# Performance work log

Measured on AMD Instinct MI355X. Metric: run time of the kernel, lower is better.

Reference implementation:

```python
import jax, jax.numpy as jnp
import numpy as np

C = 512        # channels
H = 8          # num_heads
GN_ATTN = 32   # GroupNorm32 groups
GN_CONV = 8    # Conv1dBlock GroupNorm groups


def _mish(x):
    return x * jnp.tanh(jax.nn.softplus(x))


def _group_norm(x, w, b, groups, eps=1e-5):
    # x: (B, C, T); normalize per group over (C//groups, T) in fp32
    B, Cc, T = x.shape
    xf = x.astype(jnp.float32).reshape(B, groups, Cc // groups, T)
    mean = xf.mean(axis=(2, 3), keepdims=True)
    var = xf.var(axis=(2, 3), keepdims=True)
    xn = ((xf - mean) * jax.lax.rsqrt(var + eps)).reshape(B, Cc, T)
    return (xn * w[None, :, None] + b[None, :, None]).astype(x.dtype)


def _conv1d_same(x, w, b):
    # x: (B, Cin, T), w: (Cout, Cin, K)
    y = jax.lax.conv_general_dilated(
        x, w, window_strides=(1,), padding='SAME',
        dimension_numbers=('NCH', 'OIH', 'NCH'))
    return y + b[None, :, None]


def setup_inputs() -> dict:
    key = jax.random.key(0)
    ks = jax.random.split(key, 12)
    B, T = 8, 1024
    s_qkv = 1.0 / np.sqrt(C * 2)
    s_proj = 1.0 / np.sqrt(C * 4)
    return {
        'x':       jax.random.normal(ks[0], (B, C, T), jnp.float32),
        'gn_w':    jnp.ones((C,), jnp.float32),
        'gn_b':    jnp.zeros((C,), jnp.float32),
        'wqkv':    jax.random.normal(ks[1], (3 * C, C, 2), jnp.float32) * s_qkv,
        'bqkv':    jnp.zeros((3 * C,), jnp.float32),
        'gnq_w':   jnp.ones((3 * C,), jnp.float32),
        'gnq_b':   jnp.zeros((3 * C,), jnp.float32),
        'wproj':   jax.random.normal(ks[2], (C, C, 4), jnp.float32) * s_proj,
        'bproj':   jnp.zeros((C,), jnp.float32),
        'gnp_w':   jnp.ones((C,), jnp.float32),
        'gnp_b':   jnp.zeros((C,), jnp.float32),
    }


def _qkv_attention(qkv):
    # qkv: (B*H, 3*dh, T)
    ch = qkv.shape[1] // 3
    q, k, v = jnp.split(qkv, 3, axis=1)
    scale = 1.0 / np.sqrt(np.sqrt(ch))
    # (bh, t, s) full score matrix, softmax in fp32 as original
    weight = jnp.einsum('bct,bcs->bts', q * scale, k * scale)
    weight = jax.nn.softmax(weight.astype(jnp.float32), axis=-1).astype(weight.dtype)
    return jnp.einsum('bts,bcs->bct', weight, v)


def reference(x, gn_w, gn_b, wqkv, bqkv, gnq_w, gnq_b, wproj, bproj, gnp_w, gnp_b):
    B, Cc, T = x.shape
    # norm -> qkv Conv1dBlock (conv -> GN(8) -> Mish)
    h = _group_norm(x, gn_w, gn_b, GN_ATTN)
    qkv = _mish(_group_norm(_conv1d_same(h, wqkv, bqkv), gnq_w, gnq_b, GN_CONV))
    # heads: (B, 3C, T) -> (B*H, 3C/H, T)
    qkv = qkv.reshape(B * H, (3 * Cc) // H, T)
    a = _qkv_attention(qkv)                       # (B*H, C/H, T)
    a = a.reshape(B, Cc, T)
    # proj Conv1dBlock + residual
    h = _mish(_group_norm(_conv1d_same(a, wproj, bproj), gnp_w, gnp_b, GN_CONV))
    return x + h
```

## Files before the change

kernel.cpp:

```cpp
#include <hip/hip_runtime.h>
#include <hip/hip_bf16.h>
#include <math.h>

#define TID threadIdx.x

constexpr int Cc = 512, Tt = 1024, C3 = 1536;

typedef __attribute__((ext_vector_type(8))) __bf16 bf16x8;
typedef __attribute__((ext_vector_type(4))) float f32x4;

__device__ __forceinline__ void async16(const void* g, void* l) {
  __builtin_amdgcn_global_load_lds(
      (const __attribute__((address_space(1))) unsigned int*)g,
      (__attribute__((address_space(3))) unsigned int*)l, 16, 0, 0);
}

__device__ __forceinline__ unsigned int pack2bf(float a, float b) {
  __hip_bfloat162 h;
  h.x = __float2bfloat16(a);
  h.y = __float2bfloat16(b);
  return *reinterpret_cast<unsigned int*>(&h);
}

__device__ __forceinline__ float bf2f(unsigned short u) {
  unsigned int t = ((unsigned int)u) << 16;
  union { unsigned int i; float f; } c;
  c.i = t;
  return c.f;
}

__device__ __forceinline__ float exp2_hw(float x) {
  float r;
  asm("v_exp_f32 %0, %1" : "=v"(r) : "v"(x));
  return r;
}

__device__ __forceinline__ float mishf(float x) {
  float u = __expf(x);
  float n = u * (u + 2.f);
  float r = x * n * __builtin_amdgcn_rcpf(n + 2.f);
  return (x > 20.f) ? x : r;
}

__device__ __forceinline__ void blockReduce2(float& s, float& ss) {
  #pragma unroll
  for (int off = 32; off > 0; off >>= 1) {
    s  += __shfl_xor(s,  off);
    ss += __shfl_xor(ss, off);
  }
  __shared__ float ls[4], lss[4];
  int w = TID >> 6;
  if ((TID & 63) == 0) { ls[w] = s; lss[w] = ss; }
  __syncthreads();
  s  = ls[0] + ls[1] + ls[2] + ls[3];
  ss = lss[0] + lss[1] + lss[2] + lss[3];
}

__global__ void zero_stats(float* p) { p[TID] = 0.f; }

__global__ __launch_bounds__(256) void zero_pads(__hip_bfloat16* __restrict__ aT) {
  int idx = blockIdx.x * 256 + TID;
  int bb = idx >> 11;
  int task = idx & 2047;
  int prow = task >> 6;
  int col = (task & 63) * 8;
  int P = (prow < 16) ? prow : (1024 + prow);
  uint4 z = {0u, 0u, 0u, 0u};
  *reinterpret_cast<uint4*>(aT + ((size_t)bb * 1056 + P) * 512 + col) = z;
}

__global__ __launch_bounds__(256) void gn1_hT(const float* __restrict__ x,
    const float* __restrict__ w, const float* __restrict__ bv,
    __hip_bfloat16* __restrict__ hT) {
  __shared__ float hs[16][262];
  int blk = blockIdx.x, bb = blk >> 5, g = blk & 31;
  size_t base = ((size_t)bb * Cc + g * 16) * Tt;
  const float* xp = x + base;
  float s = 0.f, ss = 0.f;
  for (int i = TID * 4; i < 16 * Tt; i += 1024) {
    float4 v = *reinterpret_cast<const float4*>(xp + i);
    s  += v.x + v.y + v.z + v.w;
    ss += v.x * v.x + v.y * v.y + v.z * v.z + v.w * v.w;
  }
  blockReduce2(s, ss);
  float mean = s * (1.f / 16384.f);
  float rstd = rsqrtf(ss * (1.f / 16384.f) - mean * mean + 1e-5f);

  __hip_bfloat16* ob = hT + (size_t)bb * 1056 * 512 + g * 16;
  for (int tc = 0; tc < 4; ++tc) {
    int tbase = tc * 256;
    __syncthreads();
    for (int task = TID; task < 1024; task += 256) {
      int row = task >> 6, c4 = task & 63;
      int ch = g * 16 + row;
      float sw = w[ch] * rstd;
      float sb = bv[ch] - mean * sw;
      float4 v = *reinterpret_cast<const float4*>(xp + (size_t)row * Tt + tbase + c4 * 4);
      hs[row][c4 * 4 + 0] = v.x * sw + sb;
      hs[row][c4 * 4 + 1] = v.y * sw + sb;
      hs[row][c4 * 4 + 2] = v.z * sw + sb;
      hs[row][c4 * 4 + 3] = v.w * sw + sb;
    }
    __syncthreads();
    for (int task = TID; task < 512; task += 256) {
      int t = task >> 1, half = task & 1;
      int c0 = half * 8;
      uint4 u;
      u.x = pack2bf(hs[c0 + 0][t], hs[c0 + 1][t]);
      u.y = pack2bf(hs[c0 + 2][t], hs[c0 + 3][t]);
      u.z = pack2bf(hs[c0 + 4][t], hs[c0 + 5][t]);
      u.w = pack2bf(hs[c0 + 6][t], hs[c0 + 7][t]);
      *reinterpret_cast<uint4*>(ob + (size_t)(16 + tbase + t) * 512 + c0) = u;
    }
  }
}

__global__ __launch_bounds__(256) void cast_wqkv(const float* __restrict__ wq,
    __hip_bfloat16* __restrict__ A1s) {
  int o = blockIdx.x;
  int ci = TID * 2;
  float4 v = *reinterpret_cast<const float4*>(wq + ((size_t)o * 512 + ci) * 2);
  unsigned int u0 = pack2bf(v.x, v.z);
  unsigned int u1 = pack2bf(v.y, v.w);
  *reinterpret_cast<unsigned int*>(A1s + (size_t)o * 512 + ci) = u0;
  *reinterpret_cast<unsigned int*>(A1s + ((size_t)1536 + o) * 512 + ci) = u1;
}

__global__ __launch_bounds__(256) void cast_wproj(const float* __restrict__ wp,
    __hip_bfloat16* __restrict__ A2) {
  int o = blockIdx.x;
  int ci = TID * 2;
  float4 v0 = *reinterpret_cast<const float4*>(wp + ((size_t)o * 512 + ci) * 4);
  float4 v1 = *reinterpret_cast<const float4*>(wp + ((size_t)o * 512 + ci + 1) * 4);
  const float* a0 = &v0.x;
  const float* a1 = &v1.x;
  #pragma unroll
  for (int j = 0; j < 4; ++j) {
    unsigned int u = pack2bf(a0[j], a1[j]);
    *reinterpret_cast<unsigned int*>(A2 + ((size_t)j * 512 + o) * 512 + ci) = u;
  }
}

__global__ __launch_bounds__(1024, 4) void gemm_s2(const __hip_bfloat16* __restrict__ A1s,
    const __hip_bfloat16* __restrict__ hT, const float* __restrict__ bias,
    __hip_bfloat16* __restrict__ Cout, float* __restrict__ statraw) {
  constexpr int BUF = 41 * 1024;
  __shared__ __align__(16) char lds[2 * BUF];
  int bz = blockIdx.x & 7;
  int inner = blockIdx.x >> 3;
  int t0 = (inner & 3) * 256;
  int og = inner >> 2;
  int o0 = og * 192;
  int wave = TID >> 6, lane = TID & 63;
  int l4 = lane >> 4, r15 = lane & 15;
  int wm = wave >> 2, wn = wave & 3;
  const __hip_bfloat16* hTb = hT + (size_t)bz * 1056 * 512;

  f32x4 acc[3][4];
  f32x4 zz = {0.f, 0.f, 0.f, 0.f};
  #pragma unroll
  for (int m = 0; m < 3; ++m)
    #pragma unroll
    for (int n = 0; n < 4; ++n) acc[m][n] = zz;

  auto stage = [&](int kt, int buf) {
    char* dst = lds + buf * BUF;
    #pragma unroll
    for (int c = 0; c < 3; ++c) {
      int ch = c * 16 + wave;
      if (ch < 41) {
        const __hip_bfloat16* src;
        if (ch < 24) {
          int j = (ch >= 12) ? 1 : 0;
          int rg = ch - j * 12;
          src = A1s + ((size_t)j * 1536 + o0 + rg * 16 + r15) * 512 + kt * 32 + l4 * 8;
        } else {
          int rg = ch - 24;
          src = hTb + (size_t)(16 + t0 + rg * 16 + r15) * 512 + kt * 32 + l4 * 8;
        }
        async16(src, dst + ch * 1024 + lane * 16);
      }
    }
  };

  stage(0, 0);
  __syncthreads();
  for (int kt = 0; kt < 16; ++kt) {
    if (kt + 1 < 16) stage(kt + 1, (kt + 1) & 1);
    char* cur = lds + (kt & 1) * BUF;
    #pragma unroll
    for (int j = 0; j < 2; ++j) {
      bf16x8 af[3], bfr[4];
      #pragma unroll
      for (int m = 0; m < 3; ++m)
        af[m] = *reinterpret_cast<const bf16x8*>(cur + (j * 12 + wm * 3 + m) * 1024 + lane * 16);
      #pragma unroll
      for (int n = 0; n < 4; ++n) {
        int q = (wn * 4 + n) * 16 + r15 + j;
        bfr[n] = *reinterpret_cast<const bf16x8*>(cur + 24 * 1024 + (q >> 4) * 1024 + l4 * 256 + (q & 15) * 16);
      }
      #pragma unroll
      for (int m = 0; m < 3; ++m)
        #pragma unroll
        for (int n = 0; n < 4; ++n)
          acc[m][n] = __builtin_amdgcn_mfma_f32_16x16x32_bf16(af[m], bfr[n], acc[m][n], 0, 0, 0);
    }
    __syncthreads();
  }

  float* sred = reinterpret_cast<float*>(lds);
  #pragma unroll
  for (int m = 0; m < 3; ++m) {
    float s = 0.f, ss2 = 0.f;
    #pragma unroll
    for (int n = 0; n < 4; ++n) {
      int ocol = t0 + (wn * 4 + n) * 16 + r15;
      #pragma unroll
      for (int r = 0; r < 4; ++r) {
        int orow = o0 + (wm * 3 + m) * 16 + l4 * 4 + r;
        float v = acc[m][n][r] + bias[orow];
        Cout[((size_t)bz * C3 + orow) * 1024 + ocol] = __float2bfloat16(v);
        s += v;
        ss2 += v * v;
      }
    }
    #pragma unroll
    for (int off = 1; off < 64; off <<= 1) {
      s   += __shfl_xor(s, off);
      ss2 += __shfl_xor(ss2, off);
    }
    if (lane == 0) {
      sred[(wave * 3 + m) * 2]     = s;
      sred[(wave * 3 + m) * 2 + 1] = ss2;
    }
  }
  __syncthreads();
  if (TID == 0) {
    float S = 0.f, SS = 0.f;
    #pragma unroll
    for (int slot = 0; slot < 48; ++slot) {
      S  += sred[slot * 2];
      SS += sred[slot * 2 + 1];
    }
    int g = bz * 8 + og;
    atomicAdd(&statraw[2 * g],     S);
    atomicAdd(&statraw[2 * g + 1], SS);
  }
}

__global__ __launch_bounds__(256) void gemm_c4b(const __hip_bfloat16* __restrict__ A2,
    const __hip_bfloat16* __restrict__ aT, const float* __restrict__ bias,
    float* __restrict__ Cout, float* __restrict__ statraw) {
  constexpr int BUF = 42 * 1024;
  __shared__ __align__(16) char lds[2 * BUF];
  int bz = blockIdx.x & 7;
  int inner = blockIdx.x >> 3;
  int t0 = (inner & 7) * 128;
  int o0 = (inner >> 3) * 128;
  int wave = TID >> 6, lane = TID & 63;
  int l4 = lane >> 4, r15 = lane & 15;
  int wm = wave >> 1, wn = wave & 1;
  const __hip_bfloat16* aTb = aT + (size_t)bz * 1056 * 512;

  f32x4 acc[4][4];
  f32x4 zz = {0.f, 0.f, 0.f, 0.f};
  #pragma unroll
  for (int m = 0; m < 4; ++m)
    #pragma unroll
    for (int n = 0; n < 4; ++n) acc[m][n] = zz;

  auto stage = [&](int kt, int buf) {
    char* dst = lds + buf * BUF;
    #pragma unroll
    for (int c = 0; c < 11; ++c) {
      int ch = c * 4 + wave;
      if (ch < 42) {
        const __hip_bfloat16* src;
        if (ch < 32) {
          int j = ch >> 3, rg = ch & 7;
          src = A2 + ((size_t)j * 512 + o0 + rg * 16 + r15) * 512 + kt * 32 + l4 * 8;
        } else {
          int rg = ch - 32;
          src = aTb + (size_t)(t0 + rg * 16 + r15) * 512 + kt * 32 + l4 * 8;
        }
        async16(src, dst + ch * 1024 + lane * 16);
      }
    }
  };

  stage(0, 0);
  __syncthreads();
  for (int kt = 0; kt < 16; ++kt) {
    if (kt + 1 < 16) stage(kt + 1, (kt + 1) & 1);
    char* cur = lds + (kt & 1) * BUF;
    #pragma unroll
    for (int j = 0; j < 4; ++j) {
      bf16x8 af[4], bfr[4];
      #pragma unroll
      for (int m = 0; m < 4; ++m)
        af[m] = *reinterpret_cast<const bf16x8*>(cur + (j * 8 + wm * 4 + m) * 1024 + lane * 16);
      #pragma unroll
      for (int n = 0; n < 4; ++n) {
        int q = (wn * 4 + n) * 16 + r15 + j + 15;
        bfr[n] = *reinterpret_cast<const bf16x8*>(cur + 32 * 1024 + (q >> 4) * 1024 + l4 * 256 + (q & 15) * 16);
      }
      #pragma unroll
      for (int m = 0; m < 4; ++m)
        #pragma unroll
        for (int n = 0; n < 4; ++n)
          acc[m][n] = __builtin_amdgcn_mfma_f32_16x16x32_bf16(af[m], bfr[n], acc[m][n], 0, 0, 0);
    }
    __syncthreads();
  }

  float* sred = reinterpret_cast<float*>(lds);
  #pragma unroll
  for (int m = 0; m < 4; ++m) {
    float s = 0.f, ss2 = 0.f;
    #pragma unroll
    for (int n = 0; n < 4; ++n) {
      int ocol = t0 + (wn * 4 + n) * 16 + r15;
      #pragma unroll
      for (int r = 0; r < 4; ++r) {
        int orow = o0 + (wm * 4 + m) * 16 + l4 * 4 + r;
        float v = acc[m][n][r] + bias[orow];
        Cout[((size_t)bz * Cc + orow) * 1024 + ocol] = v;
        s += v;
        ss2 += v * v;
      }
    }
    #pragma unroll
    for (int off = 1; off < 64; off <<= 1) {
      s   += __shfl_xor(s, off);
      ss2 += __shfl_xor(ss2, off);
    }
    if (lane == 0) {
      sred[(wave * 4 + m) * 2]     = s;
      sred[(wave * 4 + m) * 2 + 1] = ss2;
    }
  }
  __syncthreads();
  if (TID < 2) {
    int g0 = o0 >> 6;
    float S = 0.f, SS = 0.f;
    int cnt = 0;
    #pragma unroll
    for (int slot = 0; slot < 16; ++slot) {
      int rc = ((slot >> 3) << 2) + (slot & 3);
      int g = (o0 + rc * 16) >> 6;
      if (g == g0 + (int)TID) {
        S  += sred[slot * 2];
        SS += sred[slot * 2 + 1];
        ++cnt;
      }
    }
    if (cnt) {
      atomicAdd(&statraw[2 * (bz * 8 + g0 + TID)],     S);
      atomicAdd(&statraw[2 * (bz * 8 + g0 + TID) + 1], SS);
    }
  }
}

__global__ __launch_bounds__(256) void gn2_prep(const __hip_bfloat16* __restrict__ qkv,
    const float* __restrict__ straw, const float* __restrict__ w, const float* __restrict__ bv,
    char* __restrict__ qTp, char* __restrict__ kimg, char* __restrict__ vimg) {
  __shared__ unsigned short hbf[192 * 66];
  int tl = blockIdx.x & 15, hb = blockIdx.x >> 4;
  int b = hb >> 3, hd = hb & 7;
  float rs = straw[2 * (b * 8 + hd)], rq = straw[2 * (b * 8 + hd) + 1];
  float mean = rs * (1.f / 196608.f);
  float rstd = rsqrtf(fmaxf(rq * (1.f / 196608.f) - mean * mean, 0.f) + 1e-5f);
  for (int task = TID; task < 768; task += 256) {
    int row = task >> 2, seg = task & 3;
    int ch = hd * 192 + row;
    float sw = w[ch] * rstd;
    float sb = bv[ch] - mean * sw;
    const uint4* src = reinterpret_cast<const uint4*>(
        qkv + ((size_t)(b * C3 + ch)) * 1024 + tl * 64 + seg * 16);
    uint4 u0 = src[0], u1 = src[1];
    unsigned int uu[8] = {u0.x, u0.y, u0.z, u0.w, u1.x, u1.y, u1.z, u1.w};
    unsigned int* dst = reinterpret_cast<unsigned int*>(&hbf[row * 66 + seg * 16]);
    #pragma unroll
    for (int j = 0; j < 8; ++j) {
      float a = mishf(bf2f((unsigned short)(uu[j] & 0xffff)) * sw + sb);
      float c = mishf(bf2f((unsigned short)(uu[j] >> 16)) * sw + sb);
      dst[j] = pack2bf(a, c);
    }
  }
  __syncthreads();
  size_t tileof = ((size_t)hb * 16 + tl) * 8192;
  {
    int t = TID & 63, sel = TID >> 6;
    int img = sel >> 1, half = sel & 1;
    char* obase = (img == 0 ? qTp : kimg) + tileof + (size_t)t * 128;
    #pragma unroll
    for (int cc = 0; cc < 4; ++cc) {
      int chunk = half * 4 + cc;
      uint4 u;
      unsigned int* up = reinterpret_cast<unsigned int*>(&u);
      #pragma unroll
      for (int j = 0; j < 4; ++j) {
        int c = chunk * 8 + j * 2;
        unsigned int lo = hbf[(img * 64 + c) * 66 + t];
        unsigned int hi = hbf[(img * 64 + c + 1) * 66 + t];
        up[j] = lo | (hi << 16);
      }
      int cpos = (img == 0) ? chunk : (chunk ^ (t & 7));
      *reinterpret_cast<uint4*>(obase + cpos * 16) = u;
    }
  }
  {
    int c = TID & 63, qtr = TID >> 6;
    const unsigned int* vrow = reinterpret_cast<const unsigned int*>(&hbf[(128 + c) * 66]);
    char* obase = vimg + tileof + (size_t)c * 128;
    #pragma unroll
    for (int k = 0; k < 2; ++k) {
      int chunk = qtr * 2 + k;
      uint4 u;
      unsigned int* up = reinterpret_cast<unsigned int*>(&u);
      #pragma unroll
      for (int j = 0; j < 4; ++j) up[j] = vrow[chunk * 4 + j];
      *reinterpret_cast<uint4*>(obase + (chunk ^ (c & 7)) * 16) = u;
    }
  }
}

__global__ __launch_bounds__(1024) void attn_mfma6(const char* __restrict__ qTp,
    const char* __restrict__ kimg, const char* __restrict__ vimg,
    __hip_bfloat16* __restrict__ aT) {
  __shared__ __align__(16) char smem[131072];
  char* kbuf0 = smem;
  char* kbuf1 = smem + 16384;
  char* vbuf0 = smem + 32768;
  char* vbuf1 = smem + 49152;
  char* pp    = smem + 65536;
  char* ov    = smem;

  int hb = blockIdx.y;
  int b = hb >> 3, hd = hb & 7;
  int lane = TID & 63, wave = TID >> 6;
  int qt = wave >> 2, qw = wave & 3;
  int l4 = lane >> 4, r15 = lane & 15;
  size_t ibase = (size_t)hb * 16 * 8192;
  const char* ksrc = kimg + ibase;
  const char* vsrc = vimg + ibase;

  async16(ksrc + (size_t)TID * 16, kbuf0 + (size_t)TID * 16);
  async16(vsrc + (size_t)TID * 16, vbuf0 + (size_t)TID * 16);

  bf16x8 aq[2];
  int tg = qw * 16 + r15;
  const char* qrow = qTp + ibase + (size_t)(blockIdx.x * 4 + qt) * 8192 + (size_t)tg * 128;
  aq[0] = *reinterpret_cast<const bf16x8*>(qrow + l4 * 16);
  aq[1] = *reinterpret_cast<const bf16x8*>(qrow + 64 + l4 * 16);
  {
    const float SC = 0.125f * 1.44269504f;
    #pragma unroll
    for (int kk = 0; kk < 2; ++kk) {
      unsigned int* u = reinterpret_cast<unsigned int*>(&aq[kk]);
      #pragma unroll
      for (int j = 0; j < 4; ++j) {
        float lo = bf2f((unsigned short)(u[j] & 0xffff)) * SC;
        float hi = bf2f((unsigned short)(u[j] >> 16)) * SC;
        u[j] = pack2bf(lo, hi);
      }
    }
  }

  f32x4 osum[4];
  f32x4 zz = {0.f, 0.f, 0.f, 0.f};
  #pragma unroll
  for (int cf = 0; cf < 4; ++cf) osum[cf] = zz;
  float mrow[4] = {-1e30f, -1e30f, -1e30f, -1e30f};
  float lrow[4] = {0.f, 0.f, 0.f, 0.f};
  __syncthreads();

  for (int it = 0; it < 8; ++it) {
    char* kcur = (it & 1) ? kbuf1 : kbuf0;
    char* vcur = (it & 1) ? vbuf1 : vbuf0;
    if (it < 7) {
      char* knxt = (it & 1) ? kbuf0 : kbuf1;
      char* vnxt = (it & 1) ? vbuf0 : vbuf1;
      const char* kn = ksrc + (size_t)(it + 1) * 16384;
      const char* vn = vsrc + (size_t)(it + 1) * 16384;
      async16(kn + (size_t)TID * 16, knxt + (size_t)TID * 16);
      async16(vn + (size_t)TID * 16, vnxt + (size_t)TID * 16);
    }
    f32x4 sc[8];
    #pragma unroll
    for (int sf = 0; sf < 8; ++sf) sc[sf] = zz;
    #pragma unroll
    for (int sf = 0; sf < 8; ++sf) {
      int sr = sf * 16 + r15;
      #pragma unroll
      for (int kk = 0; kk < 2; ++kk) {
        bf16x8 bk = *reinterpret_cast<const bf16x8*>(kcur + sr * 128 + (((kk * 4 + l4) ^ (sr & 7)) << 4));
        sc[sf] = __builtin_amdgcn_mfma_f32_16x16x32_bf16(aq[kk], bk, sc[sf], 0, 0, 0);
      }
    }
    float tmax[4];
    #pragma unroll
    for (int r = 0; r < 4; ++r) {
      float m0 = fmaxf(fmaxf(sc[0][r], sc[1][r]), fmaxf(sc[2][r], sc[3][r]));
      float m1 = fmaxf(fmaxf(sc[4][r], sc[5][r]), fmaxf(sc[6][r], sc[7][r]));
      tmax[r] = fmaxf(m0, m1);
    }
    #pragma unroll
    for (int off = 1; off < 16; off <<= 1)
      #pragma unroll
      for (int r = 0; r < 4; ++r) tmax[r] = fmaxf(tmax[r], __shfl_xor(tmax[r], off));
    bool grow = (tmax[0] > mrow[0]) | (tmax[1] > mrow[1]) |
                (tmax[2] > mrow[2]) | (tmax[3] > mrow[3]);
    if (grow) {
      float alpha[4];
      #pragma unroll
      for (int r = 0; r < 4; ++r) {
        float mnew = fmaxf(mrow[r], tmax[r]);
        alpha[r] = exp2_hw(mrow[r] - mnew);
        mrow[r] = mnew;
        lrow[r] *= alpha[r];
      }
      #pragma unroll
      for (int cf = 0; cf < 4; ++cf)
        #pragma unroll
        for (int r = 0; r < 4; ++r) osum[cf][r] *= alpha[r];
    }
    char* pw = pp + wave * 4096;
    float psum[4] = {0.f, 0.f, 0.f, 0.f};
    #pragma unroll
    for (int sf = 0; sf < 8; ++sf) {
      int s = sf * 16 + r15;
      int chunk = s >> 3;
      #pragma unroll
      for (int r = 0; r < 4; ++r) {
        float p = exp2_hw(sc[sf][r] - mrow[r]);
        psum[r] += p;
        int tlc = l4 * 4 + r;
        *reinterpret_cast<__hip_bfloat16*>(pw + tlc * 256 + (((chunk ^ (tlc & 15)) << 4) | ((s & 7) * 2)))
            = __float2bfloat16(p);
      }
    }
    #pragma unroll
    for (int r = 0; r < 4; ++r) lrow[r] += psum[r];
    asm volatile("s_waitcnt lgkmcnt(0)" ::: "memory");
    __builtin_amdgcn_sched_barrier(0);

    bf16x8 pa[4];
    #pragma unroll
    for (int kk2 = 0; kk2 < 4; ++kk2)
      pa[kk2] = *reinterpret_cast<const bf16x8*>(pw + r15 * 256 + (((kk2 * 4 + l4) ^ (r15 & 15)) << 4));
    #pragma unroll
    for (int cf = 0; cf < 4; ++cf) {
      int cr = cf * 16 + r15;
      #pragma unroll
      for (int kk2 = 0; kk2 < 4; ++kk2) {
        bf16x8 bv = *reinterpret_cast<const bf16x8*>(vcur + (kk2 >> 1) * 8192 + cr * 128 +
                                                     ((((kk2 & 1) * 4 + l4) ^ (cr & 7)) << 4));
        osum[cf] = __builtin_amdgcn_mfma_f32_16x16x32_bf16(pa[kk2], bv, osum[cf], 0, 0, 0);
      }
    }
    __syncthreads();
  }

  #pragma unroll
  for (int off = 1; off < 16; off <<= 1)
    #pragma unroll
    for (int r = 0; r < 4; ++r) lrow[r] += __shfl_xor(lrow[r], off);
  float linv[4];
  #pragma unroll
  for (int r = 0; r < 4; ++r) linv[r] = 1.f / lrow[r];

  #pragma unroll
  for (int cf = 0; cf < 4; ++cf) {
    int c = cf * 16 + r15;
    #pragma unroll
    for (int r = 0; r < 4; ++r) {
      int t = qt * 64 + qw * 16 + l4 * 4 + r;
      *reinterpret_cast<__hip_bfloat16*>(ov + t * 128 + ((((c >> 3) ^ (t & 7)) << 4) | ((c & 7) * 2)))
          = __float2bfloat16(osum[cf][r] * linv[r]);
    }
  }
  __syncthreads();
  __hip_bfloat16* ap = aT + ((size_t)b * 1056 + 16 + blockIdx.x * 256) * 512 + hd * 64;
  for (int u = TID; u < 2048; u += 1024) {
    int t = u >> 3, cj = u & 7;
    uint4 o4 = *reinterpret_cast<const uint4*>(ov + t * 128 + ((cj ^ (t & 7)) << 4));
    *reinterpret_cast<uint4*>(ap + (size_t)t * 512 + cj * 8) = o4;
  }
}

__global__ __launch_bounds__(256) void final_kernel(const float* __restrict__ x,
    float* __restrict__ y, const float* __restrict__ straw,
    const float* __restrict__ w, const float* __restrict__ bv) {
  size_t i = ((size_t)blockIdx.x * 256 + TID) * 4;
  int ch = (int)((i >> 10) & (Cc - 1));
  int b = (int)(i >> 19);
  int g = b * 8 + (ch >> 6);
  float rs = straw[2 * g], rq = straw[2 * g + 1];
  float mean = rs * (1.f / 65536.f);
  float rstd = rsqrtf(fmaxf(rq * (1.f / 65536.f) - mean * mean, 0.f) + 1e-5f);
  float sw = w[ch] * rstd;
  float sb = bv[ch] - mean * sw;
  float4 v  = *reinterpret_cast<const float4*>(y + i);
  float4 xv = *reinterpret_cast<const float4*>(x + i);
  v.x = xv.x + mishf(v.x * sw + sb);
  v.y = xv.y + mishf(v.y * sw + sb);
  v.z = xv.z + mishf(v.z * sw + sb);
  v.w = xv.w + mishf(v.w * sw + sb);
  *reinterpret_cast<float4*>(y + i) = v;
}

extern "C" void kernel_launch(void* const* d_in, const int* in_sizes, int n_in,
                              void* d_out, int out_size, void* d_ws, size_t ws_size,
                              hipStream_t stream) {
  const float* x     = (const float*)d_in[0];
  const float* gn_w  = (const float*)d_in[1];
  const float* gn_b  = (const float*)d_in[2];
  const float* wqkv  = (const float*)d_in[3];
  const float* bqkv  = (const float*)d_in[4];
  const float* gnq_w = (const float*)d_in[5];
  const float* gnq_b = (const float*)d_in[6];
  const float* wproj = (const float*)d_in[7];
  const float* bproj = (const float*)d_in[8];
  const float* gnp_w = (const float*)d_in[9];
  const float* gnp_b = (const float*)d_in[10];
  float* out = (float*)d_out;

  char* ws = (char*)d_ws;
  const size_t MB = 1024 * 1024;
  __hip_bfloat16* qkvb = (__hip_bfloat16*)ws;
  __hip_bfloat16* aT   = (__hip_bfloat16*)(ws + 24 * MB);
  __hip_bfloat16* A1s  = (__hip_bfloat16*)(ws + 40 * MB);
  __hip_bfloat16* A2   = (__hip_bfloat16*)(ws + 44 * MB);
  char* vimg = ws + 56 * MB;
  float* st2raw = (float*)(ws + 64 * MB);
  float* st3raw = st2raw + 128;
  __hip_bfloat16* hT = (__hip_bfloat16*)d_out;
  char* qTp  = (char*)d_out;
  char* kimg = (char*)d_out + 8 * MB;

  dim3 blk(256);
  zero_stats<<<1, blk, 0, stream>>>(st2raw);
  zero_pads<<<64, blk, 0, stream>>>(aT);
  zero_pads<<<64, blk, 0, stream>>>(hT);
  cast_wqkv<<<1536, blk, 0, stream>>>(wqkv, A1s);
  gn1_hT<<<256, blk, 0, stream>>>(x, gn_w, gn_b, hT);
  gemm_s2<<<256, dim3(1024), 0, stream>>>(A1s, hT, bqkv, qkvb, st2raw);
  gn2_prep<<<1024, blk, 0, stream>>>(qkvb, st2raw, gnq_w, gnq_b, qTp, kimg, vimg);
  attn_mfma6<<<dim3(4, 64), dim3(1024), 0, stream>>>(qTp, kimg, vimg, aT);
  cast_wproj<<<512, blk, 0, stream>>>(wproj, A2);
  gemm_c4b<<<256, blk, 0, stream>>>(A2, aT, bproj, out, st3raw);
  final_kernel<<<4096, blk, 0, stream>>>(x, out, st3raw, gnp_w, gnp_b);
}
```

Before: 155.5 us.

## Merge prep kernels, retile projection GEMM, add MFMA priority hints in attention

After: 144.0 us. 1.08x faster.

```diff
diff --git a/kernel.cpp b/kernel.cpp
--- a/kernel.cpp
+++ b/kernel.cpp
@@ -56,17 +56,44 @@
   ss = lss[0] + lss[1] + lss[2] + lss[3];
 }
 
-__global__ void zero_stats(float* p) { p[TID] = 0.f; }
-
-__global__ __launch_bounds__(256) void zero_pads(__hip_bfloat16* __restrict__ aT) {
-  int idx = blockIdx.x * 256 + TID;
-  int bb = idx >> 11;
-  int task = idx & 2047;
-  int prow = task >> 6;
-  int col = (task & 63) * 8;
-  int P = (prow < 16) ? prow : (1024 + prow);
-  uint4 z = {0u, 0u, 0u, 0u};
-  *reinterpret_cast<uint4*>(aT + ((size_t)bb * 1056 + P) * 512 + col) = z;
+__global__ __launch_bounds__(256) void prep_misc(const float* __restrict__ wq,
+    const float* __restrict__ wp, __hip_bfloat16* __restrict__ A1s,
+    __hip_bfloat16* __restrict__ A2, __hip_bfloat16* __restrict__ aT,
+    __hip_bfloat16* __restrict__ hT, float* __restrict__ stats) {
+  int bid = blockIdx.x;
+  if (bid < 128) {
+    __hip_bfloat16* dst = (bid < 64) ? aT : hT;
+    int idx = ((bid & 63)) * 256 + TID;
+    int bb = idx >> 11;
+    int task = idx & 2047;
+    int prow = task >> 6;
+    int col = (task & 63) * 8;
+    int P = (prow < 16) ? prow : (1024 + prow);
+    uint4 z = {0u, 0u, 0u, 0u};
+    *reinterpret_cast<uint4*>(dst + ((size_t)bb * 1056 + P) * 512 + col) = z;
+  } else if (bid < 1664) {
+    int o = bid - 128;
+    int ci = TID * 2;
+    float4 v = *reinterpret_cast<const float4*>(wq + ((size_t)o * 512 + ci) * 2);
+    unsigned int u0 = pack2bf(v.x, v.z);
+    unsigned int u1 = pack2bf(v.y, v.w);
+    *reinterpret_cast<unsigned int*>(A1s + (size_t)o * 512 + ci) = u0;
+    *reinterpret_cast<unsigned int*>(A1s + ((size_t)1536 + o) * 512 + ci) = u1;
+  } else if (bid < 2176) {
+    int o = bid - 1664;
+    int ci = TID * 2;
+    float4 v0 = *reinterpret_cast<const float4*>(wp + ((size_t)o * 512 + ci) * 4);
+    float4 v1 = *reinterpret_cast<const float4*>(wp + ((size_t)o * 512 + ci + 1) * 4);
+    const float* a0 = &v0.x;
+    const float* a1 = &v1.x;
+    #pragma unroll
+    for (int j = 0; j < 4; ++j) {
+      unsigned int u = pack2bf(a0[j], a1[j]);
+      *reinterpret_cast<unsigned int*>(A2 + ((size_t)j * 512 + o) * 512 + ci) = u;
+    }
+  } else {
+    stats[TID] = 0.f;
+  }
 }
 
 __global__ __launch_bounds__(256) void gn1_hT(const float* __restrict__ x,
@@ -115,32 +142,6 @@
   }
 }
 
-__global__ __launch_bounds__(256) void cast_wqkv(const float* __restrict__ wq,
-    __hip_bfloat16* __restrict__ A1s) {
-  int o = blockIdx.x;
-  int ci = TID * 2;
-  float4 v = *reinterpret_cast<const float4*>(wq + ((size_t)o * 512 + ci) * 2);
-  unsigned int u0 = pack2bf(v.x, v.z);
-  unsigned int u1 = pack2bf(v.y, v.w);
-  *reinterpret_cast<unsigned int*>(A1s + (size_t)o * 512 + ci) = u0;
-  *reinterpret_cast<unsigned int*>(A1s + ((size_t)1536 + o) * 512 + ci) = u1;
-}
-
-__global__ __launch_bounds__(256) void cast_wproj(const float* __restrict__ wp,
-    __hip_bfloat16* __restrict__ A2) {
-  int o = blockIdx.x;
-  int ci = TID * 2;
-  float4 v0 = *reinterpret_cast<const float4*>(wp + ((size_t)o * 512 + ci) * 4);
-  float4 v1 = *reinterpret_cast<const float4*>(wp + ((size_t)o * 512 + ci + 1) * 4);
-  const float* a0 = &v0.x;
-  const float* a1 = &v1.x;
-  #pragma unroll
-  for (int j = 0; j < 4; ++j) {
-    unsigned int u = pack2bf(a0[j], a1[j]);
-    *reinterpret_cast<unsigned int*>(A2 + ((size_t)j * 512 + o) * 512 + ci) = u;
-  }
-}
-
 __global__ __launch_bounds__(1024, 4) void gemm_s2(const __hip_bfloat16* __restrict__ A1s,
     const __hip_bfloat16* __restrict__ hT, const float* __restrict__ bias,
     __hip_bfloat16* __restrict__ Cout, float* __restrict__ statraw) {
@@ -248,18 +249,17 @@
   }
 }
 
-__global__ __launch_bounds__(256) void gemm_c4b(const __hip_bfloat16* __restrict__ A2,
+__global__ __launch_bounds__(256) void gemm_c4d(const __hip_bfloat16* __restrict__ A2,
     const __hip_bfloat16* __restrict__ aT, const float* __restrict__ bias,
     float* __restrict__ Cout, float* __restrict__ statraw) {
-  constexpr int BUF = 42 * 1024;
+  constexpr int BUF = 34 * 1024;
   __shared__ __align__(16) char lds[2 * BUF];
   int bz = blockIdx.x & 7;
   int inner = blockIdx.x >> 3;
-  int t0 = (inner & 7) * 128;
-  int o0 = (inner >> 3) * 128;
+  int t0 = (inner & 3) * 256;
+  int o0 = (inner >> 2) * 64;
   int wave = TID >> 6, lane = TID & 63;
   int l4 = lane >> 4, r15 = lane & 15;
-  int wm = wave >> 1, wn = wave & 1;
   const __hip_bfloat16* aTb = aT + (size_t)bz * 1056 * 512;
 
   f32x4 acc[4][4];
@@ -272,15 +272,15 @@
   auto stage = [&](int kt, int buf) {
     char* dst = lds + buf * BUF;
     #pragma unroll
-    for (int c = 0; c < 11; ++c) {
+    for (int c = 0; c < 9; ++c) {
       int ch = c * 4 + wave;
-      if (ch < 42) {
+      if (ch < 34) {
         const __hip_bfloat16* src;
-        if (ch < 32) {
-          int j = ch >> 3, rg = ch & 7;
+        if (ch < 16) {
+          int j = ch >> 2, rg = ch & 3;
           src = A2 + ((size_t)j * 512 + o0 + rg * 16 + r15) * 512 + kt * 32 + l4 * 8;
         } else {
-          int rg = ch - 32;
+          int rg = ch - 16;
           src = aTb + (size_t)(t0 + rg * 16 + r15) * 512 + kt * 32 + l4 * 8;
         }
         async16(src, dst + ch * 1024 + lane * 16);
@@ -298,11 +298,11 @@
       bf16x8 af[4], bfr[4];
       #pragma unroll
       for (int m = 0; m < 4; ++m)
-        af[m] = *reinterpret_cast<const bf16x8*>(cur + (j * 8 + wm * 4 + m) * 1024 + lane * 16);
+        af[m] = *reinterpret_cast<const bf16x8*>(cur + (j * 4 + m) * 1024 + lane * 16);
       #pragma unroll
       for (int n = 0; n < 4; ++n) {
-        int q = (wn * 4 + n) * 16 + r15 + j + 15;
-        bfr[n] = *reinterpret_cast<const bf16x8*>(cur + 32 * 1024 + (q >> 4) * 1024 + l4 * 256 + (q & 15) * 16);
+        int q = (wave * 4 + n) * 16 + r15 + j + 15;
+        bfr[n] = *reinterpret_cast<const bf16x8*>(cur + 16 * 1024 + (q >> 4) * 1024 + l4 * 256 + (q & 15) * 16);
       }
       #pragma unroll
       for (int m = 0; m < 4; ++m)
@@ -319,10 +319,10 @@
     float s = 0.f, ss2 = 0.f;
     #pragma unroll
     for (int n = 0; n < 4; ++n) {
-      int ocol = t0 + (wn * 4 + n) * 16 + r15;
+      int ocol = t0 + (wave * 4 + n) * 16 + r15;
       #pragma unroll
       for (int r = 0; r < 4; ++r) {
-        int orow = o0 + (wm * 4 + m) * 16 + l4 * 4 + r;
+        int orow = o0 + m * 16 + l4 * 4 + r;
         float v = acc[m][n][r] + bias[orow];
         Cout[((size_t)bz * Cc + orow) * 1024 + ocol] = v;
         s += v;
@@ -340,24 +340,16 @@
     }
   }
   __syncthreads();
-  if (TID < 2) {
-    int g0 = o0 >> 6;
+  if (TID == 0) {
     float S = 0.f, SS = 0.f;
-    int cnt = 0;
     #pragma unroll
     for (int slot = 0; slot < 16; ++slot) {
-      int rc = ((slot >> 3) << 2) + (slot & 3);
-      int g = (o0 + rc * 16) >> 6;
-      if (g == g0 + (int)TID) {
-        S  += sred[slot * 2];
-        SS += sred[slot * 2 + 1];
-        ++cnt;
-      }
-    }
-    if (cnt) {
-      atomicAdd(&statraw[2 * (bz * 8 + g0 + TID)],     S);
-      atomicAdd(&statraw[2 * (bz * 8 + g0 + TID) + 1], SS);
-    }
+      S  += sred[slot * 2];
+      SS += sred[slot * 2 + 1];
+    }
+    int g = bz * 8 + (o0 >> 6);
+    atomicAdd(&statraw[2 * g],     S);
+    atomicAdd(&statraw[2 * g + 1], SS);
   }
 }
 
@@ -489,6 +481,7 @@
     f32x4 sc[8];
     #pragma unroll
     for (int sf = 0; sf < 8; ++sf) sc[sf] = zz;
+    __builtin_amdgcn_s_setprio(1);
     #pragma unroll
     for (int sf = 0; sf < 8; ++sf) {
       int sr = sf * 16 + r15;
@@ -498,6 +491,7 @@
         sc[sf] = __builtin_amdgcn_mfma_f32_16x16x32_bf16(aq[kk], bk, sc[sf], 0, 0, 0);
       }
     }
+    __builtin_amdgcn_s_setprio(0);
     float tmax[4];
     #pragma unroll
     for (int r = 0; r < 4; ++r) {
@@ -549,6 +543,7 @@
     #pragma unroll
     for (int kk2 = 0; kk2 < 4; ++kk2)
       pa[kk2] = *reinterpret_cast<const bf16x8*>(pw + r15 * 256 + (((kk2 * 4 + l4) ^ (r15 & 15)) << 4));
+    __builtin_amdgcn_s_setprio(1);
     #pragma unroll
     for (int cf = 0; cf < 4; ++cf) {
       int cr = cf * 16 + r15;
@@ -559,6 +554,7 @@
         osum[cf] = __builtin_amdgcn_mfma_f32_16x16x32_bf16(pa[kk2], bv, osum[cf], 0, 0, 0);
       }
     }
+    __builtin_amdgcn_s_setprio(0);
     __syncthreads();
   }
 
@@ -640,15 +636,11 @@
   char* kimg = (char*)d_out + 8 * MB;
 
   dim3 blk(256);
-  zero_stats<<<1, blk, 0, stream>>>(st2raw);
-  zero_pads<<<64, blk, 0, stream>>>(aT);
-  zero_pads<<<64, blk, 0, stream>>>(hT);
-  cast_wqkv<<<1536, blk, 0, stream>>>(wqkv, A1s);
+  prep_misc<<<2177, blk, 0, stream>>>(wqkv, wproj, A1s, A2, aT, hT, st2raw);
   gn1_hT<<<256, blk, 0, stream>>>(x, gn_w, gn_b, hT);
   gemm_s2<<<256, dim3(1024), 0, stream>>>(A1s, hT, bqkv, qkvb, st2raw);
   gn2_prep<<<1024, blk, 0, stream>>>(qkvb, st2raw, gnq_w, gnq_b, qTp, kimg, vimg);
   attn_mfma6<<<dim3(4, 64), dim3(1024), 0, stream>>>(qTp, kimg, vimg, aT);
-  cast_wproj<<<512, blk, 0, stream>>>(wproj, A2);
-  gemm_c4b<<<256, blk, 0, stream>>>(A2, aT, bproj, out, st3raw);
+  gemm_c4d<<<256, blk, 0, stream>>>(A2, aT, bproj, out, st3raw);
   final_kernel<<<4096, blk, 0, stream>>>(x, out, st3raw, gnp_w, gnp_b);
 }
```
